# Kernel optimization log

Hardware: AMD Instinct MI355X
Metric: run time of the kernel (lower is better)

## Reference

```python
import jax, jax.numpy as jnp
import numpy as np

THRESH = 0.3
LENS = 0.5

@jax.custom_vjp
def spike_fn(x):
    return (x > 0).astype(x.dtype)

def _spike_fwd(x):
    return spike_fn(x), x

def _spike_bwd(x, g):
    # boxcar surrogate gradient: 1/(2*lens) for |x| < lens
    return (g * (jnp.abs(x) < LENS).astype(g.dtype) / (2.0 * LENS),)

spike_fn.defvjp(_spike_fwd, _spike_bwd)


def setup_inputs() -> dict:
    key = jax.random.key(0)
    ks = jax.random.split(key, 9)
    B, T, N_in, H, O = 256, 64, 700, 2048, 20
    s_ih = 1.0 / np.sqrt(N_in)
    s_hh = 1.0 / np.sqrt(H)
    s_ho = 1.0 / np.sqrt(H)
    return {
        "input": jax.random.uniform(ks[0], (B, T, N_in), dtype=jnp.float32),
        "W_ih": jax.random.normal(ks[1], (H, N_in), dtype=jnp.float32) * s_ih,
        "b_ih": jax.random.normal(ks[2], (H,), dtype=jnp.float32) * s_ih,
        "W_hh": jax.random.normal(ks[3], (H, H), dtype=jnp.float32) * s_hh,
        "b_hh": jax.random.normal(ks[4], (H,), dtype=jnp.float32) * s_hh,
        "W_ho": jax.random.normal(ks[5], (O, H), dtype=jnp.float32) * s_ho,
        "b_ho": jax.random.normal(ks[6], (O,), dtype=jnp.float32) * s_ho,
        "tau_m_h": jnp.full((1,), 20.0, dtype=jnp.float32),
        "tau_m_o": jnp.full((1,), 20.0, dtype=jnp.float32),
    }


def reference(input, W_ih, b_ih, W_hh, b_hh, W_ho, b_ho, tau_m_h, tau_m_o):
    B, T, _ = input.shape
    H = W_ih.shape[0]
    O = W_ho.shape[0]
    alpha_h = jnp.exp(-1.0 / tau_m_h)  # [1], broadcasts over [B, H]
    alpha_o = jnp.exp(-1.0 / tau_m_o)

    # Precompute input projection for all steps: [T, B, H]
    x_proj = jnp.einsum("bti,hi->tbh", input, W_ih) + b_ih

    def step(carry, xp):
        h_mem, h_spike, o_mem, o_spike, o_sum = carry
        # recurrent LIF hidden update
        h_mem = h_mem * alpha_h * (1.0 - h_spike) + xp + h_spike @ W_hh.T + b_hh
        h_spike = spike_fn(h_mem - THRESH)
        # output LIF update
        o_mem = o_mem * alpha_o * (1.0 - o_spike) + h_spike @ W_ho.T + b_ho
        o_spike = spike_fn(o_mem - THRESH)
        o_sum = o_sum + o_spike
        return (h_mem, h_spike, o_mem, o_spike, o_sum), None

    zH = jnp.zeros((B, H), dtype=input.dtype)
    zO = jnp.zeros((B, O), dtype=input.dtype)
    (_, _, _, _, o_sumspike), _ = jax.lax.scan(step, (zH, zH, zO, zO, zO), x_proj)
    return o_sumspike / T
```

## Files before the change

kernel.cpp:

```cpp
#include <hip/hip_runtime.h>
#include <stdint.h>

typedef __attribute__((ext_vector_type(4))) int i32x4;

static constexpr int BB = 256, TT = 64, NIN = 700, NKP = 768, HH = 2048, OO = 20;
static constexpr float THRESH_V = 0.3f;
static constexpr int NBLK = 256;
static constexpr int NREC = 16;
static constexpr int XNIT = 11;
static constexpr int NIT  = NREC + XNIT;

static constexpr size_t OFF_HMEM  = 0;
static constexpr size_t OFF_SPK0  = 2097152;
static constexpr size_t OFF_OMEM  = 2621440;
static constexpr size_t OFF_OSPK  = 2641920;
static constexpr size_t OFF_OSUM  = 2662400;
static constexpr size_t ZERO_END  = 2682880;
static constexpr size_t OFF_SPK1  = 2682880;
static constexpr size_t OFF_ALPHA = 3207168;
static constexpr size_t OFF_WHHD  = 3207424;
static constexpr size_t WHH_PLANE = 4194304;
static constexpr size_t OFF_WIHD  = 19984640;
static constexpr size_t WIH_PLANE = 1572864;
static constexpr size_t OFF_XD    = 26276096;
static constexpr size_t XD_PLANE  = 12582912;
static constexpr size_t WS_NEED   = 76607744;
#define WAIT_VM12() asm volatile("s_waitcnt vmcnt(12)" ::: "memory")
#define WAIT_VM6()  asm volatile("s_waitcnt vmcnt(6)" ::: "memory")
#define WAIT_VM0()  asm volatile("s_waitcnt vmcnt(0)" ::: "memory")
#define SCHED0()    __builtin_amdgcn_sched_barrier(0)

__device__ __forceinline__ void wdig(float w, double scale, signed char d[4]) {
    int q = (int)rint((double)w * scale);
    int t0 = (int)(signed char)(q & 0xFF); q = (q - t0) >> 8;
    int t1 = (int)(signed char)(q & 0xFF); q = (q - t1) >> 8;
    int t2 = (int)(signed char)(q & 0xFF); q = (q - t2) >> 8;
    d[0] = (signed char)t0; d[1] = (signed char)t1;
    d[2] = (signed char)t2; d[3] = (signed char)q;
}

__device__ __forceinline__ i32x4 ld_rec(const uint8_t* base, int row, int sl) {
    return *reinterpret_cast<const i32x4*>(base + row * 128 + ((sl ^ (row & 7)) << 4));
}
__device__ __forceinline__ i32x4 ld_x(const uint8_t* base, int row, int s) {
    int phys = (s + (row >> 1)) & 3;
    return *reinterpret_cast<const i32x4*>(base + row * 64 + (phys << 4));
}

__device__ __forceinline__ void gload(const uint8_t* src, uint8_t* dst) {
    __builtin_amdgcn_global_load_lds((const __attribute__((address_space(1))) void*)src,
                                     (__attribute__((address_space(3))) void*)dst, 16, 0, 0);
}

__device__ __forceinline__ void stage_rec(uint8_t* buf, const int8_t* spk, const int8_t* whhd,
                                          int m0, int n0, int k0B, int wid, int lane) {
#pragma unroll
    for (int i = 0; i < 2; ++i) {
        int c   = wid + i * 4;
        int row = c * 8 + (lane >> 3);
        int s   = (lane & 7) ^ (row & 7);
        gload((const uint8_t*)spk + (size_t)(m0 + row) * HH + k0B + (s << 4),
              buf + c * 1024);
    }
#pragma unroll
    for (int sub = 0; sub < 4; ++sub) {
        int row = sub * 8 + (lane >> 3);
        int s   = (lane & 7) ^ (row & 7);
        gload((const uint8_t*)whhd + (size_t)wid * WHH_PLANE +
              (size_t)(n0 + row) * HH + k0B + (s << 4),
              buf + 8192 + wid * 4096 + sub * 1024);
    }
}
__device__ __forceinline__ void stage_x(uint8_t* buf, const int8_t* xd_t, const int8_t* wihd,
                                        int m0, int n0, int k0B, int wid, int lane) {
#pragma unroll
    for (int sub = 0; sub < 4; ++sub) {
        int row = sub * 16 + (lane >> 2);
        int s   = ((lane & 3) - (row >> 1)) & 3;
        gload((const uint8_t*)xd_t + (size_t)wid * XD_PLANE +
              (size_t)(m0 + row) * NKP + k0B + (s << 4),
              buf + wid * 4096 + sub * 1024);
    }
#pragma unroll
    for (int i = 0; i < 2; ++i) {
        int cb  = wid + i * 4;
        int p   = cb >> 1, sub = cb & 1;
        int row = sub * 16 + (lane >> 2);
        int s   = ((lane & 3) - (row >> 1)) & 3;
        gload((const uint8_t*)wihd + (size_t)p * WIH_PLANE +
              (size_t)(n0 + row) * NKP + k0B + (s << 4),
              buf + 16384 + p * 2048 + sub * 1024);
    }
}

__device__ __forceinline__ void mfma_rec(const uint8_t* buf, int mw, int nw, int fr, int hi4,
                                         i32x4 aR[4][2]) {
#pragma unroll
    for (int ks = 0; ks < 2; ++ks) {
        int sl = ks * 4 + hi4;
        i32x4 a0 = ld_rec(buf, mw * 32 + fr,      sl);
        i32x4 a1 = ld_rec(buf, mw * 32 + 16 + fr, sl);
#pragma unroll
        for (int p = 0; p < 4; ++p) {
            i32x4 b = ld_rec(buf + 8192 + p * 4096, nw * 16 + fr, sl);
            aR[p][0] = __builtin_amdgcn_mfma_i32_16x16x64_i8(a0, b, aR[p][0], 0, 0, 0);
            aR[p][1] = __builtin_amdgcn_mfma_i32_16x16x64_i8(a1, b, aR[p][1], 0, 0, 0);
        }
    }
}
__device__ __forceinline__ void mfma_x(const uint8_t* buf, int mw, int nw, int fr, int hi4,
                                       i32x4 aX[5][2]) {
    i32x4 fa[4][2], fb[4];
#pragma unroll
    for (int p = 0; p < 4; ++p) {
        fa[p][0] = ld_x(buf + p * 4096, mw * 32 + fr,      hi4);
        fa[p][1] = ld_x(buf + p * 4096, mw * 32 + 16 + fr, hi4);
        fb[p]    = ld_x(buf + 16384 + p * 2048, nw * 16 + fr, hi4);
    }
#pragma unroll
    for (int a = 0; a < 4; ++a)
#pragma unroll
        for (int b = 0; b < 4; ++b) {
            if (a + b < 2) continue;
            const int c = a + b - 2;
            aX[c][0] = __builtin_amdgcn_mfma_i32_16x16x64_i8(fa[a][0], fb[b], aX[c][0], 0, 0, 0);
            aX[c][1] = __builtin_amdgcn_mfma_i32_16x16x64_i8(fa[a][1], fb[b], aX[c][1], 0, 0, 0);
        }
}

__global__ __launch_bounds__(256) void conv_whh_i8(const float* __restrict__ W,
                                                   int8_t* __restrict__ p0, int8_t* __restrict__ p1,
                                                   int8_t* __restrict__ p2, int8_t* __restrict__ p3,
                                                   const float* __restrict__ tau_h,
                                                   const float* __restrict__ tau_o,
                                                   float* __restrict__ alpha) {
    int idx = blockIdx.x * 256 + threadIdx.x;
    if (idx == 0) {
        float qh = __fdiv_rn(-1.0f, tau_h[0]);
        float qo = __fdiv_rn(-1.0f, tau_o[0]);
        alpha[0] = (float)exp((double)qh);
        alpha[1] = (float)exp((double)qo);
    }
    float4 v = reinterpret_cast<const float4*>(W)[idx];
    signed char dx[4], dy[4], dz[4], dw[4];
    const double SC = 1073741824.0;
    wdig(v.x, SC, dx); wdig(v.y, SC, dy); wdig(v.z, SC, dz); wdig(v.w, SC, dw);
    reinterpret_cast<char4*>(p0)[idx] = make_char4(dx[0], dy[0], dz[0], dw[0]);
    reinterpret_cast<char4*>(p1)[idx] = make_char4(dx[1], dy[1], dz[1], dw[1]);
    reinterpret_cast<char4*>(p2)[idx] = make_char4(dx[2], dy[2], dz[2], dw[2]);
    reinterpret_cast<char4*>(p3)[idx] = make_char4(dx[3], dy[3], dz[3], dw[3]);
}

__global__ __launch_bounds__(256) void conv_wih_i8(const float* __restrict__ W,
                                                   int8_t* __restrict__ p0, int8_t* __restrict__ p1,
                                                   int8_t* __restrict__ p2, int8_t* __restrict__ p3) {
    int row = blockIdx.x;
    for (int i = threadIdx.x; i < NKP; i += 256) {
        float v = (i < NIN) ? W[(size_t)row * NIN + i] : 0.f;
        signed char d[4];
        wdig(v, 1073741824.0, d);
        size_t o = (size_t)row * NKP + i;
        p0[o] = d[0]; p1[o] = d[1]; p2[o] = d[2]; p3[o] = d[3];
    }
}

__global__ __launch_bounds__(256) void conv_x_i8(const float* __restrict__ in,
                                                 int8_t* __restrict__ p0, int8_t* __restrict__ p1,
                                                 int8_t* __restrict__ p2, int8_t* __restrict__ p3) {
    int blk = blockIdx.x;
    int t = blk >> 8, b = blk & 255;
    const float* src = in + ((size_t)b * TT + t) * NIN;
    size_t dst = ((size_t)t * BB + b) * NKP;
    for (int i = threadIdx.x; i < NKP; i += 256) {
        float v = (i < NIN) ? src[i] : 0.f;
        signed char d[4];
        wdig(v, 16777216.0, d);
        p0[dst + i] = d[0]; p1[dst + i] = d[1]; p2[dst + i] = d[2]; p3[dst + i] = d[3];
    }
}

__device__ __forceinline__ void odot_block(int g, int wid, int lane, const int8_t* __restrict__ spk,
                                           const float* __restrict__ W_ho,
                                           const float* __restrict__ b_ho,
                                           float a_o, float* __restrict__ o_mem,
                                           float* __restrict__ o_spk, float* __restrict__ o_sum,
                                           float* __restrict__ out ) {
    const int8_t* srow = spk + (size_t)g * HH + lane * 32;
    int4 s0 = *reinterpret_cast<const int4*>(srow);
    int4 s1 = *reinterpret_cast<const int4*>(srow + 16);
    int sw[8] = {s0.x, s0.y, s0.z, s0.w, s1.x, s1.y, s1.z, s1.w};
#pragma unroll 1
    for (int p = 0; p < 5; ++p) {
        int o = wid * 5 + p;
        const float* wrow = W_ho + (size_t)o * HH + lane * 32;
        double acc = 0.0;
#pragma unroll
        for (int q = 0; q < 8; ++q) {
            float4 w = *reinterpret_cast<const float4*>(wrow + q * 4);
            int sv = sw[q];
            acc += (sv & 0x000000FF) ? (double)w.x : 0.0;
            acc += (sv & 0x0000FF00) ? (double)w.y : 0.0;
            acc += (sv & 0x00FF0000) ? (double)w.z : 0.0;
            acc += (sv & 0xFF000000) ? (double)w.w : 0.0;
        }
#pragma unroll
        for (int off = 32; off >= 1; off >>= 1)
            acc += __shfl_xor(acc, off, 64);
        if (lane == 0) {
            float dot = (float)acc;
            size_t oo = (size_t)g * OO + o;
            float om = o_mem[oo], osp = o_spk[oo];
            float v = __fadd_rn(__fadd_rn(__fmul_rn(__fmul_rn(om, a_o), 1.f - osp), dot), b_ho[o]);
            float sn = (v > THRESH_V) ? 1.f : 0.f;
            o_mem[oo] = v;
            o_spk[oo] = sn;
            float s = __fadd_rn(o_sum[oo], sn);
            o_sum[oo] = s;
            if (out) out[oo] = __fmul_rn(s, 1.f / 64.f);
        }
    }
}

__global__ __launch_bounds__(256) void step_kernel(
    const int8_t* __restrict__ whhd, const int8_t* __restrict__ wihd,
    const int8_t* __restrict__ xd,
    const int8_t* __restrict__ spk_rd, int8_t* __restrict__ spk_wr,
    float* __restrict__ h_mem, const float* __restrict__ alpha,
    const float* __restrict__ b_ih, const float* __restrict__ b_hh,
    const float* __restrict__ W_ho, const float* __restrict__ b_ho,
    float* __restrict__ o_mem, float* __restrict__ o_spk, float* __restrict__ o_sum,
    int t) {
    __shared__ __align__(16) uint8_t L0[24576];
    __shared__ __align__(16) uint8_t L1[24576];
    __shared__ __align__(16) uint8_t L2[24576];
    __shared__ __align__(16) uint8_t L3[24576];

    int g   = blockIdx.x;
    int tid = threadIdx.x;
    int lane = tid & 63, wid = tid >> 6;
    int m0 = (g >> 6) * 64;
    int n0 = (g & 63) * 32;
    int mw = wid >> 1, nw = wid & 1;
    int fr = lane & 15, hi4 = lane >> 4;

    const int8_t* xd_t = xd + (size_t)t * BB * NKP;

    i32x4 aR[4][2] = {};
    i32x4 aX[5][2] = {};

    stage_rec(L0, spk_rd, whhd, m0, n0, 0,   wid, lane);
    stage_rec(L1, spk_rd, whhd, m0, n0, 128, wid, lane);
    stage_rec(L2, spk_rd, whhd, m0, n0, 256, wid, lane);

#pragma unroll
    for (int h = 0; h < NIT; ++h) {
        if (h <= NIT - 3) { WAIT_VM12(); }
        else if (h == NIT - 2) { WAIT_VM6(); }
        else { WAIT_VM0(); }
        SCHED0();
        __builtin_amdgcn_s_barrier();
        if (h + 3 < NIT) {
            uint8_t* nb = ((h + 3) & 3) == 0 ? L0 : ((h + 3) & 3) == 1 ? L1
                        : ((h + 3) & 3) == 2 ? L2 : L3;
            int c = h + 3;
            if (c < NREC) stage_rec(nb, spk_rd, whhd, m0, n0, c * 128, wid, lane);
            else          stage_x(nb, xd_t, wihd, m0, n0, (c - NREC) * 64, wid, lane);
        }
        const uint8_t* cb = (h & 3) == 0 ? L0 : (h & 3) == 1 ? L1
                          : (h & 3) == 2 ? L2 : L3;
        __builtin_amdgcn_s_setprio(1);
        if (h < NREC) mfma_rec(cb, mw, nw, fr, hi4, aR);
        else          mfma_x(cb, mw, nw, fr, hi4, aX);
        __builtin_amdgcn_s_setprio(0);
    }

    float a_h = alpha[0];
    int j  = n0 + nw * 16 + fr;
    int rq = hi4 * 4;
#pragma unroll
    for (int msub = 0; msub < 2; ++msub)
#pragma unroll
        for (int rr = 0; rr < 4; ++rr) {
            int b = m0 + mw * 32 + msub * 16 + rq + rr;
            size_t off = (size_t)b * HH + j;
            float recf = (float)((double)aR[3][msub][rr] * 0x1p-6
                               + (double)aR[2][msub][rr] * 0x1p-14
                               + (double)aR[1][msub][rr] * 0x1p-22
                               + (double)aR[0][msub][rr] * 0x1p-30);
            double xp64 = (double)aX[4][msub][rr] * 0x1p-6
                        + (double)aX[3][msub][rr] * 0x1p-14
                        + (double)aX[2][msub][rr] * 0x1p-22
                        + (double)aX[1][msub][rr] * 0x1p-30
                        + (double)aX[0][msub][rr] * 0x1p-38;
            float xpf = (float)xp64;
            float xpb = __fadd_rn(xpf, b_ih[j]);
            float hv  = h_mem[off];
            float keep = spk_rd[off] ? 0.f : 1.f;
            float v = __fadd_rn(__fmul_rn(__fmul_rn(hv, a_h), keep), xpb);
            v = __fadd_rn(v, recf);
            v = __fadd_rn(v, b_hh[j]);
            h_mem[off] = v;
            spk_wr[off] = (v > THRESH_V) ? (int8_t)1 : (int8_t)0;
        }

    if (t > 0)
        odot_block(g, wid, lane, spk_rd, W_ho, b_ho, alpha[1], o_mem, o_spk, o_sum, nullptr);
}

__global__ __launch_bounds__(256) void final_kernel(const int8_t* __restrict__ spk,
                                                    const float* __restrict__ W_ho,
                                                    const float* __restrict__ b_ho,
                                                    const float* __restrict__ alpha,
                                                    float* __restrict__ o_mem,
                                                    float* __restrict__ o_spk,
                                                    float* __restrict__ o_sum,
                                                    float* __restrict__ out) {
    int lane = threadIdx.x & 63, wid = threadIdx.x >> 6;
    odot_block(blockIdx.x, wid, lane, spk, W_ho, b_ho, alpha[1], o_mem, o_spk, o_sum, out);
}

extern "C" void kernel_launch(void* const* d_in, const int* in_sizes, int n_in,
                              void* d_out, int out_size, void* d_ws, size_t ws_size,
                              hipStream_t stream) {
    const float* in    = (const float*)d_in[0];
    const float* W_ih  = (const float*)d_in[1];
    const float* b_ih  = (const float*)d_in[2];
    const float* W_hh  = (const float*)d_in[3];
    const float* b_hh  = (const float*)d_in[4];
    const float* W_ho  = (const float*)d_in[5];
    const float* b_ho  = (const float*)d_in[6];
    const float* tau_h = (const float*)d_in[7];
    const float* tau_o = (const float*)d_in[8];

    uint8_t* ws = (uint8_t*)d_ws;
    float*  h_mem = (float*)(ws + OFF_HMEM);
    int8_t* spk0  = (int8_t*)(ws + OFF_SPK0);
    float*  o_mem = (float*)(ws + OFF_OMEM);
    float*  o_spk = (float*)(ws + OFF_OSPK);
    float*  o_sum = (float*)(ws + OFF_OSUM);
    int8_t* spk1  = (int8_t*)(ws + OFF_SPK1);
    float*  alpha = (float*)(ws + OFF_ALPHA);
    int8_t* whhd  = (int8_t*)(ws + OFF_WHHD);
    int8_t* wihd  = (int8_t*)(ws + OFF_WIHD);
    int8_t* xd    = (int8_t*)(ws + OFF_XD);

    if (ws_size < WS_NEED) return;

    hipMemsetAsync(ws, 0, ZERO_END, stream);
    conv_whh_i8<<<4096, 256, 0, stream>>>(W_hh,
                                          whhd, whhd + WHH_PLANE, whhd + 2 * WHH_PLANE, whhd + 3 * WHH_PLANE,
                                          tau_h, tau_o, alpha);
    conv_wih_i8<<<2048, 256, 0, stream>>>(W_ih,
                                          wihd, wihd + WIH_PLANE, wihd + 2 * WIH_PLANE, wihd + 3 * WIH_PLANE);
    conv_x_i8<<<16384, 256, 0, stream>>>(in,
                                         xd, xd + XD_PLANE, xd + 2 * XD_PLANE, xd + 3 * XD_PLANE);

    for (int t = 0; t < TT; ++t) {
        const int8_t* srd = (t & 1) ? spk1 : spk0;
        int8_t*       swr = (t & 1) ? spk0 : spk1;
        step_kernel<<<NBLK, 256, 0, stream>>>(whhd, wihd, xd, srd, swr, h_mem, alpha,
                                              b_ih, b_hh, W_ho, b_ho,
                                              o_mem, o_spk, o_sum, t);
    }
    final_kernel<<<NBLK, 256, 0, stream>>>(spk0, W_ho, b_ho, alpha, o_mem, o_spk, o_sum,
                                           (float*)d_out);
}
```

Before: 1.541 ms.

## Double step kernel to eight waves, each owning a 16-row MFMA sub-tile

Raises the step and final kernels from 256 to 512 threads, so each wave computes one 16x16 output fragment instead of two. The staging loads are redistributed across eight waves (three loads each), and the vmcnt waits are adjusted to match. The output dot product is spread over eight waves. The goal is more waves per CU to hide latency in the per-timestep recurrent GEMM, at the cost of more barrier participants and less register-level reuse of B fragments.

```diff
diff --git a/kernel.cpp b/kernel.cpp
--- a/kernel.cpp
+++ b/kernel.cpp
@@ -25,8 +25,9 @@
 static constexpr size_t OFF_XD    = 26276096;
 static constexpr size_t XD_PLANE  = 12582912;
 static constexpr size_t WS_NEED   = 76607744;
-#define WAIT_VM12() asm volatile("s_waitcnt vmcnt(12)" ::: "memory")
+
 #define WAIT_VM6()  asm volatile("s_waitcnt vmcnt(6)" ::: "memory")
+#define WAIT_VM3()  asm volatile("s_waitcnt vmcnt(3)" ::: "memory")
 #define WAIT_VM0()  asm volatile("s_waitcnt vmcnt(0)" ::: "memory")
 #define SCHED0()    __builtin_amdgcn_sched_barrier(0)
 
@@ -55,67 +56,66 @@
 __device__ __forceinline__ void stage_rec(uint8_t* buf, const int8_t* spk, const int8_t* whhd,
                                           int m0, int n0, int k0B, int wid, int lane) {
 #pragma unroll
-    for (int i = 0; i < 2; ++i) {
-        int c   = wid + i * 4;
-        int row = c * 8 + (lane >> 3);
-        int s   = (lane & 7) ^ (row & 7);
-        gload((const uint8_t*)spk + (size_t)(m0 + row) * HH + k0B + (s << 4),
-              buf + c * 1024);
-    }
-#pragma unroll
-    for (int sub = 0; sub < 4; ++sub) {
-        int row = sub * 8 + (lane >> 3);
-        int s   = (lane & 7) ^ (row & 7);
-        gload((const uint8_t*)whhd + (size_t)wid * WHH_PLANE +
-              (size_t)(n0 + row) * HH + k0B + (s << 4),
-              buf + 8192 + wid * 4096 + sub * 1024);
+    for (int i = 0; i < 3; ++i) {
+        int u = wid * 3 + i;
+        if (u < 8) {
+            int row = u * 8 + (lane >> 3);
+            int s   = (lane & 7) ^ (row & 7);
+            gload((const uint8_t*)spk + (size_t)(m0 + row) * HH + k0B + (s << 4),
+                  buf + u * 1024);
+        } else {
+            int v = u - 8, p = v >> 2, sub = v & 3;
+            int row = sub * 8 + (lane >> 3);
+            int s   = (lane & 7) ^ (row & 7);
+            gload((const uint8_t*)whhd + (size_t)p * WHH_PLANE +
+                  (size_t)(n0 + row) * HH + k0B + (s << 4),
+                  buf + 8192 + p * 4096 + sub * 1024);
+        }
     }
 }
 __device__ __forceinline__ void stage_x(uint8_t* buf, const int8_t* xd_t, const int8_t* wihd,
                                         int m0, int n0, int k0B, int wid, int lane) {
 #pragma unroll
-    for (int sub = 0; sub < 4; ++sub) {
-        int row = sub * 16 + (lane >> 2);
-        int s   = ((lane & 3) - (row >> 1)) & 3;
-        gload((const uint8_t*)xd_t + (size_t)wid * XD_PLANE +
-              (size_t)(m0 + row) * NKP + k0B + (s << 4),
-              buf + wid * 4096 + sub * 1024);
-    }
-#pragma unroll
-    for (int i = 0; i < 2; ++i) {
-        int cb  = wid + i * 4;
-        int p   = cb >> 1, sub = cb & 1;
-        int row = sub * 16 + (lane >> 2);
-        int s   = ((lane & 3) - (row >> 1)) & 3;
-        gload((const uint8_t*)wihd + (size_t)p * WIH_PLANE +
-              (size_t)(n0 + row) * NKP + k0B + (s << 4),
-              buf + 16384 + p * 2048 + sub * 1024);
+    for (int i = 0; i < 3; ++i) {
+        int u = wid * 3 + i;
+        if (u < 16) {
+            int p = u >> 2, sub = u & 3;
+            int row = sub * 16 + (lane >> 2);
+            int s   = ((lane & 3) - (row >> 1)) & 3;
+            gload((const uint8_t*)xd_t + (size_t)p * XD_PLANE +
+                  (size_t)(m0 + row) * NKP + k0B + (s << 4),
+                  buf + p * 4096 + sub * 1024);
+        } else {
+            int v = u - 16, p = v >> 1, sub = v & 1;
+            int row = sub * 16 + (lane >> 2);
+            int s   = ((lane & 3) - (row >> 1)) & 3;
+            gload((const uint8_t*)wihd + (size_t)p * WIH_PLANE +
+                  (size_t)(n0 + row) * NKP + k0B + (s << 4),
+                  buf + 16384 + p * 2048 + sub * 1024);
+        }
     }
 }
 
 __device__ __forceinline__ void mfma_rec(const uint8_t* buf, int mw, int nw, int fr, int hi4,
-                                         i32x4 aR[4][2]) {
+                                         i32x4 aR[4]) {
 #pragma unroll
     for (int ks = 0; ks < 2; ++ks) {
         int sl = ks * 4 + hi4;
-        i32x4 a0 = ld_rec(buf, mw * 32 + fr,      sl);
-        i32x4 a1 = ld_rec(buf, mw * 32 + 16 + fr, sl);
+        i32x4 a = ld_rec(buf, mw * 16 + fr, sl);
 #pragma unroll
         for (int p = 0; p < 4; ++p) {
             i32x4 b = ld_rec(buf + 8192 + p * 4096, nw * 16 + fr, sl);
-            aR[p][0] = __builtin_amdgcn_mfma_i32_16x16x64_i8(a0, b, aR[p][0], 0, 0, 0);
-            aR[p][1] = __builtin_amdgcn_mfma_i32_16x16x64_i8(a1, b, aR[p][1], 0, 0, 0);
+            aR[p] = __builtin_amdgcn_mfma_i32_16x16x64_i8(a, b, aR[p], 0, 0, 0);
         }
     }
 }
 __device__ __forceinline__ void mfma_x(const uint8_t* buf, int mw, int nw, int fr, int hi4,
-                                       i32x4 aX[5][2]) {
-    i32x4 fa[4][2], fb[4];
+                                       i32x4 aX[5]) {
+    i32x4 fa[4], fb[4];
 #pragma unroll
     for (int p = 0; p < 4; ++p) {
-        fa[p][0] = ld_x(buf + p * 4096, mw * 32 + fr,      hi4);
-        fa[p][1] = ld_x(buf + p * 4096, mw * 32 + 16 + fr, hi4);
-        fb[p]    = ld_x(buf + 16384 + p * 2048, nw * 16 + fr, hi4);
+        fa[p] = ld_x(buf + p * 4096,         mw * 16 + fr, hi4);
+        fb[p] = ld_x(buf + 16384 + p * 2048, nw * 16 + fr, hi4);
     }
 #pragma unroll
     for (int a = 0; a < 4; ++a)
@@ -123,8 +123,7 @@
         for (int b = 0; b < 4; ++b) {
             if (a + b < 2) continue;
             const int c = a + b - 2;
-            aX[c][0] = __builtin_amdgcn_mfma_i32_16x16x64_i8(fa[a][0], fb[b], aX[c][0], 0, 0, 0);
-            aX[c][1] = __builtin_amdgcn_mfma_i32_16x16x64_i8(fa[a][1], fb[b], aX[c][1], 0, 0, 0);
+            aX[c] = __builtin_amdgcn_mfma_i32_16x16x64_i8(fa[a], fb[b], aX[c], 0, 0, 0);
         }
 }
 
@@ -190,8 +189,9 @@
     int4 s1 = *reinterpret_cast<const int4*>(srow + 16);
     int sw[8] = {s0.x, s0.y, s0.z, s0.w, s1.x, s1.y, s1.z, s1.w};
 #pragma unroll 1
-    for (int p = 0; p < 5; ++p) {
-        int o = wid * 5 + p;
+    for (int p = 0; p < 3; ++p) {
+        int o = wid + 8 * p;
+        if (o >= OO) break;
         const float* wrow = W_ho + (size_t)o * HH + lane * 32;
         double acc = 0.0;
 #pragma unroll
@@ -221,7 +221,7 @@
     }
 }
 
-__global__ __launch_bounds__(256) void step_kernel(
+__global__ __launch_bounds__(512) void step_kernel(
     const int8_t* __restrict__ whhd, const int8_t* __restrict__ wihd,
     const int8_t* __restrict__ xd,
     const int8_t* __restrict__ spk_rd, int8_t* __restrict__ spk_wr,
@@ -245,8 +245,8 @@
 
     const int8_t* xd_t = xd + (size_t)t * BB * NKP;
 
-    i32x4 aR[4][2] = {};
-    i32x4 aX[5][2] = {};
+    i32x4 aR[4] = {};
+    i32x4 aX[5] = {};
 
     stage_rec(L0, spk_rd, whhd, m0, n0, 0,   wid, lane);
     stage_rec(L1, spk_rd, whhd, m0, n0, 128, wid, lane);
@@ -254,8 +254,8 @@
 
 #pragma unroll
     for (int h = 0; h < NIT; ++h) {
-        if (h <= NIT - 3) { WAIT_VM12(); }
-        else if (h == NIT - 2) { WAIT_VM6(); }
+        if (h < NIT - 2) { WAIT_VM6(); }
+        else if (h == NIT - 2) { WAIT_VM3(); }
         else { WAIT_VM0(); }
         SCHED0();
         __builtin_amdgcn_s_barrier();
@@ -278,36 +278,34 @@
     int j  = n0 + nw * 16 + fr;
     int rq = hi4 * 4;
 #pragma unroll
-    for (int msub = 0; msub < 2; ++msub)
-#pragma unroll
-        for (int rr = 0; rr < 4; ++rr) {
-            int b = m0 + mw * 32 + msub * 16 + rq + rr;
-            size_t off = (size_t)b * HH + j;
-            float recf = (float)((double)aR[3][msub][rr] * 0x1p-6
-                               + (double)aR[2][msub][rr] * 0x1p-14
-                               + (double)aR[1][msub][rr] * 0x1p-22
-                               + (double)aR[0][msub][rr] * 0x1p-30);
-            double xp64 = (double)aX[4][msub][rr] * 0x1p-6
-                        + (double)aX[3][msub][rr] * 0x1p-14
-                        + (double)aX[2][msub][rr] * 0x1p-22
-                        + (double)aX[1][msub][rr] * 0x1p-30
-                        + (double)aX[0][msub][rr] * 0x1p-38;
-            float xpf = (float)xp64;
-            float xpb = __fadd_rn(xpf, b_ih[j]);
-            float hv  = h_mem[off];
-            float keep = spk_rd[off] ? 0.f : 1.f;
-            float v = __fadd_rn(__fmul_rn(__fmul_rn(hv, a_h), keep), xpb);
-            v = __fadd_rn(v, recf);
-            v = __fadd_rn(v, b_hh[j]);
-            h_mem[off] = v;
-            spk_wr[off] = (v > THRESH_V) ? (int8_t)1 : (int8_t)0;
-        }
+    for (int rr = 0; rr < 4; ++rr) {
+        int b = m0 + mw * 16 + rq + rr;
+        size_t off = (size_t)b * HH + j;
+        float recf = (float)((double)aR[3][rr] * 0x1p-6
+                           + (double)aR[2][rr] * 0x1p-14
+                           + (double)aR[1][rr] * 0x1p-22
+                           + (double)aR[0][rr] * 0x1p-30);
+        double xp64 = (double)aX[4][rr] * 0x1p-6
+                    + (double)aX[3][rr] * 0x1p-14
+                    + (double)aX[2][rr] * 0x1p-22
+                    + (double)aX[1][rr] * 0x1p-30
+                    + (double)aX[0][rr] * 0x1p-38;
+        float xpf = (float)xp64;
+        float xpb = __fadd_rn(xpf, b_ih[j]);
+        float hv  = h_mem[off];
+        float keep = spk_rd[off] ? 0.f : 1.f;
+        float v = __fadd_rn(__fmul_rn(__fmul_rn(hv, a_h), keep), xpb);
+        v = __fadd_rn(v, recf);
+        v = __fadd_rn(v, b_hh[j]);
+        h_mem[off] = v;
+        spk_wr[off] = (v > THRESH_V) ? (int8_t)1 : (int8_t)0;
+    }
 
     if (t > 0)
         odot_block(g, wid, lane, spk_rd, W_ho, b_ho, alpha[1], o_mem, o_spk, o_sum, nullptr);
 }
 
-__global__ __launch_bounds__(256) void final_kernel(const int8_t* __restrict__ spk,
+__global__ __launch_bounds__(512) void final_kernel(const int8_t* __restrict__ spk,
                                                     const float* __restrict__ W_ho,
                                                     const float* __restrict__ b_ho,
                                                     const float* __restrict__ alpha,
@@ -358,10 +356,10 @@
     for (int t = 0; t < TT; ++t) {
         const int8_t* srd = (t & 1) ? spk1 : spk0;
         int8_t*       swr = (t & 1) ? spk0 : spk1;
-        step_kernel<<<NBLK, 256, 0, stream>>>(whhd, wihd, xd, srd, swr, h_mem, alpha,
+        step_kernel<<<NBLK, 512, 0, stream>>>(whhd, wihd, xd, srd, swr, h_mem, alpha,
                                               b_ih, b_hh, W_ho, b_ho,
                                               o_mem, o_spk, o_sum, t);
     }
-    final_kernel<<<NBLK, 256, 0, stream>>>(spk0, W_ho, b_ho, alpha, o_mem, o_spk, o_sum,
+    final_kernel<<<NBLK, 512, 0, stream>>>(spk0, W_ho, b_ho, alpha, o_mem, o_spk, o_sum,
                                            (float*)d_out);
 }
```

Result: faster. 1.243 ms (-19.4%).
